# Performance work log

Hardware: AMD Instinct MI355X
Metric: run time of the kernel (lower is better)

The kernel has to match this reference:

```python
import jax, jax.numpy as jnp
import numpy as np

B, T, HID = 1, 2048, 4096
H, KVH, D = 32, 8, 128
N_REP = H // KVH
SCALE = D ** -0.5
EPS = 1e-6
THETA = 10000.0
TOPK, SINK, WIN = 256, 16, 256


def _rms_norm(x, w):
    var = jnp.mean(x * x, axis=-1, keepdims=True)
    return w * (x * jax.lax.rsqrt(var + EPS))


def _rotate_half(x):
    x1, x2 = x[..., : D // 2], x[..., D // 2 :]
    return jnp.concatenate([-x2, x1], axis=-1)


def setup_inputs() -> dict:
    key = jax.random.key(0)
    ks = jax.random.split(key, 6)
    hidden_states = jax.random.normal(ks[0], (B, T, HID), jnp.float32)
    Wq = jax.random.normal(ks[1], (HID, H * D), jnp.float32) * 0.02
    Wkv = jax.random.normal(ks[2], (HID, KVH * D), jnp.float32) * 0.02
    Wo = jax.random.normal(ks[3], (H * D, HID), jnp.float32) * 0.02
    q_norm_w = jnp.ones((D,), jnp.float32)
    k_norm_w = jnp.ones((D,), jnp.float32)
    # standard RoPE tables, theta=10000
    inv_freq = 1.0 / (THETA ** (jnp.arange(0, D, 2, dtype=jnp.float32) / D))
    freqs = jnp.arange(T, dtype=jnp.float32)[:, None] * inv_freq[None, :]  # (T, D/2)
    emb = jnp.concatenate([freqs, freqs], axis=-1)  # (T, D)
    cos = jnp.cos(emb)[None]  # (1, T, D)
    sin = jnp.sin(emb)[None]
    return {"hidden_states": hidden_states, "Wq": Wq, "Wkv": Wkv, "Wo": Wo,
            "q_norm_w": q_norm_w, "k_norm_w": k_norm_w, "cos": cos, "sin": sin}


def reference(hidden_states, Wq, Wkv, Wo, q_norm_w, k_norm_w, cos, sin):
    b, t, _ = hidden_states.shape
    s = t
    # projections -> (b, h, t, d)
    q = (hidden_states @ Wq).reshape(b, t, H, D).transpose(0, 2, 1, 3)
    kv = (hidden_states @ Wkv).reshape(b, t, KVH, D).transpose(0, 2, 1, 3)
    # qk RMSNorm per head_dim
    q = _rms_norm(q, q_norm_w)
    k = _rms_norm(kv, k_norm_w)
    v = kv  # latent KV: value shares the latent projection (no norm / rope)
    # rotary, cos/sin unsqueezed at head dim
    c = cos[:, None]  # (1,1,T,D)
    sn = sin[:, None]
    q = q * c + _rotate_half(q) * sn
    k = k * c + _rotate_half(k) * sn
    # GQA expansion
    k = jnp.repeat(k, N_REP, axis=1)
    v = jnp.repeat(v, N_REP, axis=1)
    # dense scores (reference path)
    scores = jnp.einsum("bhtd,bhsd->bhts", q, k) * SCALE  # (b,h,t,s)
    # ---- sparse DSA mask: sink | local window | per-query top-k, then causal ----
    q_idx = jnp.arange(t)
    k_idx = jnp.arange(s)
    sink = (k_idx < SINK)[None, None, None, :]
    local = (jnp.abs(q_idx[:, None] - k_idx[None, :]) <= WIN)[None, None]
    kth = jax.lax.top_k(scores, TOPK)[0][..., -1:]  # k-th largest per query
    topk_keep = scores >= kth
    causal_ok = (k_idx[None, :] <= q_idx[:, None])[None, None]
    keep = (sink | local | topk_keep) & causal_ok
    scores = jnp.where(keep, scores, -jnp.inf)
    attn = jax.nn.softmax(scores, axis=-1)
    out = jnp.einsum("bhts,bhsd->bhtd", attn, v)
    out = out.transpose(0, 2, 1, 3).reshape(b, t, H * D)
    return out @ Wo
```

## Files before the change

### kernel.cpp

```cpp
#include <hip/hip_runtime.h>
#include <hip/hip_bf16.h>

#define H 32
#define KVH 8
#define D 128
#define T 2048
#define HID 4096
#define TOPK 256
#define SINK 16
#define WIN 256
#define SCALE2 0.12753102600893415f
#define NPROJ 5120

#define SWZ(row, b) ((b) ^ (((row) & 7) << 4))

#define AS3(p) ((__attribute__((address_space(3))) void*)(p))
#define AS1(p) ((const __attribute__((address_space(1))) void*)(p))

typedef __attribute__((ext_vector_type(4))) float f32x4;
typedef __attribute__((ext_vector_type(8))) short short8;

__device__ __forceinline__ unsigned short f2bf(float f) {
  unsigned int b = __float_as_uint(f);
  b += 0x7FFFu + ((b >> 16) & 1u);
  return (unsigned short)(b >> 16);
}
__device__ __forceinline__ float bf2f(unsigned short u) {
  return __uint_as_float(((unsigned int)u) << 16);
}
__device__ __forceinline__ float ldf(const void* p, long i, bool b16) {
  return b16 ? bf2f(((const unsigned short*)p)[i]) : ((const float*)p)[i];
}
__device__ __forceinline__ bool bf16_mode(const unsigned int* probe) {
  return *probe == 0x3F803F80u;
}

__global__ void cvt_kernel(const void* __restrict__ src, unsigned short* __restrict__ dst,
                           long n, const unsigned int* probe) {
  bool b16 = bf16_mode(probe);
  long stride = (long)gridDim.x * blockDim.x;
  for (long i = (long)blockIdx.x * blockDim.x + threadIdx.x; i * 8 < n; i += stride) {
    long o = i * 8;
    if (b16) {
      *(uint4*)(dst + o) = *(const uint4*)((const unsigned short*)src + o);
    } else {
      const float* s = (const float*)src + o;
      float4 f0 = *(const float4*)s;
      float4 f1 = *(const float4*)(s + 4);
      uint4 v;
      v.x = (unsigned int)f2bf(f0.x) | ((unsigned int)f2bf(f0.y) << 16);
      v.y = (unsigned int)f2bf(f0.z) | ((unsigned int)f2bf(f0.w) << 16);
      v.z = (unsigned int)f2bf(f1.x) | ((unsigned int)f2bf(f1.y) << 16);
      v.w = (unsigned int)f2bf(f1.z) | ((unsigned int)f2bf(f1.w) << 16);
      *(uint4*)(dst + o) = v;
    }
  }
}

__global__ __launch_bounds__(256) void cvt_t(const void* __restrict__ src,
    unsigned short* __restrict__ dst, int R, int Cc, const unsigned int* probe) {
  __shared__ float tile[64][65];
  bool b16 = bf16_mode(probe);
  int r0 = blockIdx.y * 64, c0 = blockIdx.x * 64;
  int tid = threadIdx.x;
  int tr = tid >> 3;
  int tc8 = (tid & 7) * 8;
#pragma unroll
  for (int p = 0; p < 2; ++p) {
    int row = tr + p * 32;
    if (b16) {
      const unsigned short* s = (const unsigned short*)src + (size_t)(r0 + row) * Cc + c0 + tc8;
      uint4 d = *(const uint4*)s;
      const unsigned short* dv = (const unsigned short*)&d;
#pragma unroll
      for (int j = 0; j < 8; ++j) tile[row][tc8 + j] = bf2f(dv[j]);
    } else {
      const float* s = (const float*)src + (size_t)(r0 + row) * Cc + c0 + tc8;
      float4 f0 = *(const float4*)s;
      float4 f1 = *(const float4*)(s + 4);
      tile[row][tc8 + 0] = f0.x; tile[row][tc8 + 1] = f0.y;
      tile[row][tc8 + 2] = f0.z; tile[row][tc8 + 3] = f0.w;
      tile[row][tc8 + 4] = f1.x; tile[row][tc8 + 5] = f1.y;
      tile[row][tc8 + 6] = f1.z; tile[row][tc8 + 7] = f1.w;
    }
  }
  __syncthreads();
#pragma unroll
  for (int p = 0; p < 2; ++p) {
    int oc = tr + p * 32;
    unsigned short tmp[8];
#pragma unroll
    for (int j = 0; j < 8; ++j) tmp[j] = f2bf(tile[tc8 + j][oc]);
    *(uint4*)(dst + (size_t)(c0 + oc) * R + r0 + tc8) = *(uint4*)tmp;
  }
}

__global__ __launch_bounds__(256) void gemm_bf16(
    const unsigned short* __restrict__ A, const unsigned short* __restrict__ Bt,
    void* __restrict__ C, int M, int N, int K, const unsigned int* probe, int outmode) {
  __shared__ alignas(16) unsigned short As[128 * 32];
  __shared__ alignas(16) unsigned short Bs[128 * 32];
  int lin = blockIdx.x;
  int qq = (int)gridDim.x >> 3;
  int swz = (lin & 7) * qq + (lin >> 3);
  int nx = N >> 7;
  int n0 = (swz % nx) * 128, m0 = (swz / nx) * 128;
  int tid = threadIdx.x;
  int w = tid >> 6, l = tid & 63;
  int wm = (w >> 1) * 64, wn = (w & 1) * 64;
  int lr = l & 15, lg = l >> 4;

  int srow0 = (w * 2 + 0) * 16 + (l >> 2);
  int srow1 = (w * 2 + 1) * 16 + (l >> 2);
  int cch = l & 3;
  int sf0 = (srow0 ^ (srow0 >> 2)) & 3;
  int sf1 = (srow1 ^ (srow1 >> 2)) & 3;
  const unsigned short* gA0 = A + (size_t)(m0 + srow0) * K + ((cch ^ sf0) * 8);
  const unsigned short* gA1 = A + (size_t)(m0 + srow1) * K + ((cch ^ sf1) * 8);
  const unsigned short* gB0 = Bt + (size_t)(n0 + srow0) * K + ((cch ^ sf0) * 8);
  const unsigned short* gB1 = Bt + (size_t)(n0 + srow1) * K + ((cch ^ sf1) * 8);
  unsigned short* lA0 = As + (w * 2 + 0) * 16 * 32;
  unsigned short* lA1 = As + (w * 2 + 1) * 16 * 32;
  unsigned short* lB0 = Bs + (w * 2 + 0) * 16 * 32;
  unsigned short* lB1 = Bs + (w * 2 + 1) * 16 * 32;

  const unsigned short* pa[4];
  const unsigned short* pb[4];
#pragma unroll
  for (int i = 0; i < 4; ++i) {
    int ra = wm + i * 16 + lr;
    int fa = (ra ^ (ra >> 2)) & 3;
    pa[i] = As + ra * 32 + ((lg ^ fa) * 8);
    int rb = wn + i * 16 + lr;
    int fb = (rb ^ (rb >> 2)) & 3;
    pb[i] = Bs + rb * 32 + ((lg ^ fb) * 8);
  }

  f32x4 zero = {0.f, 0.f, 0.f, 0.f};
  f32x4 acc[4][4];
#pragma unroll
  for (int i = 0; i < 4; ++i)
#pragma unroll
    for (int j = 0; j < 4; ++j) acc[i][j] = zero;

  for (int k0 = 0; k0 < K; k0 += 32) {
    __builtin_amdgcn_global_load_lds(AS1(gA0 + k0), AS3(lA0), 16, 0, 0);
    __builtin_amdgcn_global_load_lds(AS1(gA1 + k0), AS3(lA1), 16, 0, 0);
    __builtin_amdgcn_global_load_lds(AS1(gB0 + k0), AS3(lB0), 16, 0, 0);
    __builtin_amdgcn_global_load_lds(AS1(gB1 + k0), AS3(lB1), 16, 0, 0);
    __syncthreads();
    short8 a[4], b[4];
#pragma unroll
    for (int i = 0; i < 4; ++i) {
      a[i] = *(const short8*)pa[i];
      b[i] = *(const short8*)pb[i];
    }
#pragma unroll
    for (int i = 0; i < 4; ++i)
#pragma unroll
      for (int j = 0; j < 4; ++j)
        acc[i][j] = __builtin_amdgcn_mfma_f32_16x16x32_bf16(a[i], b[j], acc[i][j], 0, 0, 0);
    __syncthreads();
  }
  bool b16out = (outmode == 1) || (outmode == 2 && bf16_mode(probe));
#pragma unroll
  for (int i = 0; i < 4; ++i)
#pragma unroll
    for (int j = 0; j < 4; ++j)
#pragma unroll
      for (int r = 0; r < 4; ++r) {
        int row = m0 + wm + i * 16 + lg * 4 + r;
        int col = n0 + wn + j * 16 + lr;
        float v = acc[i][j][r];
        if (b16out) ((unsigned short*)C)[(size_t)row * N + col] = f2bf(v);
        else ((float*)C)[(size_t)row * N + col] = v;
      }
}

__global__ __launch_bounds__(256) void gemm_qk(
    const unsigned short* __restrict__ Qall, const unsigned short* __restrict__ Kall,
    unsigned short* __restrict__ Sout, int h0) {
  __shared__ alignas(16) unsigned short As[128 * 32];
  __shared__ alignas(16) unsigned short Bs[128 * 32];
  int lin = blockIdx.x;
  int swz = (lin & 7) * 32 + (lin >> 3);
  int n0 = (swz & 15) * 128, m0 = (swz >> 4) * 128;
  int h = h0 + blockIdx.y;
  const unsigned short* A = Qall + (size_t)h * (T * D);
  const unsigned short* Bt = Kall + (size_t)(h >> 2) * (T * D);
  unsigned short* C = Sout + (size_t)blockIdx.y * T * T;
  int tid = threadIdx.x;
  int w = tid >> 6, l = tid & 63;
  int wm = (w >> 1) * 64, wn = (w & 1) * 64;
  int lr = l & 15, lg = l >> 4;

  int srow0 = (w * 2 + 0) * 16 + (l >> 2);
  int srow1 = (w * 2 + 1) * 16 + (l >> 2);
  int cch = l & 3;
  int sf0 = (srow0 ^ (srow0 >> 2)) & 3;
  int sf1 = (srow1 ^ (srow1 >> 2)) & 3;
  const unsigned short* gA0 = A + (size_t)(m0 + srow0) * D + ((cch ^ sf0) * 8);
  const unsigned short* gA1 = A + (size_t)(m0 + srow1) * D + ((cch ^ sf1) * 8);
  const unsigned short* gB0 = Bt + (size_t)(n0 + srow0) * D + ((cch ^ sf0) * 8);
  const unsigned short* gB1 = Bt + (size_t)(n0 + srow1) * D + ((cch ^ sf1) * 8);
  unsigned short* lA0 = As + (w * 2 + 0) * 16 * 32;
  unsigned short* lA1 = As + (w * 2 + 1) * 16 * 32;
  unsigned short* lB0 = Bs + (w * 2 + 0) * 16 * 32;
  unsigned short* lB1 = Bs + (w * 2 + 1) * 16 * 32;

  const unsigned short* pa[4];
  const unsigned short* pb[4];
#pragma unroll
  for (int i = 0; i < 4; ++i) {
    int ra = wm + i * 16 + lr;
    int fa = (ra ^ (ra >> 2)) & 3;
    pa[i] = As + ra * 32 + ((lg ^ fa) * 8);
    int rb = wn + i * 16 + lr;
    int fb = (rb ^ (rb >> 2)) & 3;
    pb[i] = Bs + rb * 32 + ((lg ^ fb) * 8);
  }

  f32x4 zero = {0.f, 0.f, 0.f, 0.f};
  f32x4 acc[4][4];
#pragma unroll
  for (int i = 0; i < 4; ++i)
#pragma unroll
    for (int j = 0; j < 4; ++j) acc[i][j] = zero;

#pragma unroll
  for (int k0 = 0; k0 < D; k0 += 32) {
    __builtin_amdgcn_global_load_lds(AS1(gA0 + k0), AS3(lA0), 16, 0, 0);
    __builtin_amdgcn_global_load_lds(AS1(gA1 + k0), AS3(lA1), 16, 0, 0);
    __builtin_amdgcn_global_load_lds(AS1(gB0 + k0), AS3(lB0), 16, 0, 0);
    __builtin_amdgcn_global_load_lds(AS1(gB1 + k0), AS3(lB1), 16, 0, 0);
    __syncthreads();
    short8 a[4], b[4];
#pragma unroll
    for (int i = 0; i < 4; ++i) {
      a[i] = *(const short8*)pa[i];
      b[i] = *(const short8*)pb[i];
    }
#pragma unroll
    for (int i = 0; i < 4; ++i)
#pragma unroll
      for (int j = 0; j < 4; ++j)
        acc[i][j] = __builtin_amdgcn_mfma_f32_16x16x32_bf16(a[i], b[j], acc[i][j], 0, 0, 0);
    __syncthreads();
  }
#pragma unroll
  for (int i = 0; i < 4; ++i)
#pragma unroll
    for (int j = 0; j < 4; ++j)
#pragma unroll
      for (int r = 0; r < 4; ++r) {
        int row = m0 + wm + i * 16 + lg * 4 + r;
        int col = n0 + wn + j * 16 + lr;
        C[(size_t)row * T + col] = f2bf(acc[i][j][r]);
      }
}

__global__ __launch_bounds__(256) void qk_prep(
    const unsigned short* __restrict__ Proj, const void* nw, const void* cosp, const void* sinp,
    unsigned short* __restrict__ Qh, const unsigned int* probe) {
  bool b16 = bf16_mode(probe);
  int w = threadIdx.x >> 6, l = threadIdx.x & 63;
  int gw = blockIdx.x * 4 + w;
  int t = gw >> 5, h = gw & 31;
  const unsigned short* x = Proj + (size_t)t * NPROJ + h * D;
  float x1 = bf2f(x[l]), x2 = bf2f(x[l + 64]);
  float s = x1 * x1 + x2 * x2;
  for (int m = 32; m; m >>= 1) s += __shfl_xor(s, m);
  float inv = rsqrtf(s * (1.0f / D) + 1e-6f);
  float w1 = ldf(nw, l, b16), w2 = ldf(nw, l + 64, b16);
  float c1 = ldf(cosp, (long)t * D + l, b16), c2 = ldf(cosp, (long)t * D + l + 64, b16);
  float s1 = ldf(sinp, (long)t * D + l, b16), s2 = ldf(sinp, (long)t * D + l + 64, b16);
  float xn1 = x1 * inv * w1, xn2 = x2 * inv * w2;
  unsigned short* o = Qh + (size_t)h * T * D + (size_t)t * D;
  o[l] = f2bf(SCALE2 * (xn1 * c1 - xn2 * s1));
  o[l + 64] = f2bf(SCALE2 * (xn2 * c2 + xn1 * s2));
}

__global__ __launch_bounds__(256) void kv_prep(
    const unsigned short* __restrict__ Proj, const void* nw, const void* cosp, const void* sinp,
    unsigned short* __restrict__ Kh, unsigned short* __restrict__ Vt, const unsigned int* probe) {
  bool b16 = bf16_mode(probe);
  int w = threadIdx.x >> 6, l = threadIdx.x & 63;
  int gw = blockIdx.x * 4 + w;
  int t = gw >> 3, h = gw & 7;
  const unsigned short* x = Proj + (size_t)t * NPROJ + (H * D) + h * D;
  float x1 = bf2f(x[l]), x2 = bf2f(x[l + 64]);
  Vt[(size_t)h * D * T + (size_t)l * T + t] = x[l];
  Vt[(size_t)h * D * T + (size_t)(l + 64) * T + t] = x[l + 64];
  float s = x1 * x1 + x2 * x2;
  for (int m = 32; m; m >>= 1) s += __shfl_xor(s, m);
  float inv = rsqrtf(s * (1.0f / D) + 1e-6f);
  float w1 = ldf(nw, l, b16), w2 = ldf(nw, l + 64, b16);
  float c1 = ldf(cosp, (long)t * D + l, b16), c2 = ldf(cosp, (long)t * D + l + 64, b16);
  float s1 = ldf(sinp, (long)t * D + l, b16), s2 = ldf(sinp, (long)t * D + l + 64, b16);
  float xn1 = x1 * inv * w1, xn2 = x2 * inv * w2;
  unsigned short* o = Kh + (size_t)h * T * D + (size_t)t * D;
  o[l] = f2bf(xn1 * c1 - xn2 * s1);
  o[l + 64] = f2bf(xn2 * c2 + xn1 * s2);
}

__global__ __launch_bounds__(1024, 8) void attn_sm(
    const unsigned short* __restrict__ S,
    const unsigned short* __restrict__ Vt, unsigned short* __restrict__ attn_out, int h0) {
  __shared__ alignas(16) unsigned short sc[16][2048];
  __shared__ alignas(16) float part[8][64][4];
  __shared__ float zinv[16];
  int t0 = blockIdx.x * 16;
  int h = h0 + blockIdx.y;
  int hk = h >> 2;
  int tid = threadIdx.x;
  int w = tid >> 6, l = tid & 63;
  int lr = l & 15, lg = l >> 4;
  f32x4 zero = {0.f, 0.f, 0.f, 0.f};
  char* scB = (char*)sc;

  {
    int row = w, tq = t0 + row;
    int rsw = (row & 7) << 4;
    int lim = (t0 + 15) >> 7;
    char* rb = scB + row * 4096;
    const unsigned int* Sr = (const unsigned int*)(S + ((size_t)blockIdx.y * T + tq) * T);
#pragma unroll
    for (int i = 0; i < 16; ++i)
      *(unsigned int*)(rb + ((256 * i + 4 * l) ^ rsw)) = Sr[l + 64 * i];
    unsigned int klo[16], khi[16];
#pragma unroll
    for (int i = 0; i < 16; ++i) {
      unsigned int b = *(const unsigned int*)(rb + ((256 * i + 4 * l) ^ rsw));
      unsigned int m = (b >> 15) & 0x00010001u;
      unsigned int kk2 = b ^ (0x80008000u | (m * 0x7FFFu));
      klo[i] = kk2 & 0xFFFFu;
      khi[i] = kk2 >> 16;
    }
    unsigned int um = 0;
#pragma unroll
    for (int i = 0; i < 16; ++i) {
      unsigned int a_ = klo[i] > khi[i] ? klo[i] : khi[i];
      um = um > a_ ? um : a_;
    }
    for (int m = 32; m; m >>= 1) {
      unsigned int o = (unsigned int)__shfl_xor((int)um, m);
      um = um > o ? um : o;
    }
    unsigned int lo = 0, hi = um;
    {
      unsigned int mid = um > 192u ? um - 192u : 1u;
      int cnt = 0;
#pragma unroll
      for (int i = 0; i < 16; ++i)
        cnt += (int)__popcll(__ballot(klo[i] >= mid)) + (int)__popcll(__ballot(khi[i] >= mid));
      if (cnt >= TOPK) lo = mid; else hi = mid - 1u;
    }
    if (lo == 0u && um > 1024u) {
      unsigned int mid = um - 1024u;
      int cnt = 0;
#pragma unroll
      for (int i = 0; i < 16; ++i)
        cnt += (int)__popcll(__ballot(klo[i] >= mid)) + (int)__popcll(__ballot(khi[i] >= mid));
      if (cnt >= TOPK) lo = mid; else hi = mid - 1u;
    }
    while (lo < hi) {
      unsigned int mid = (lo + hi + 1u) >> 1;
      int cnt = 0;
#pragma unroll
      for (int i = 0; i < 16; ++i)
        cnt += (int)__popcll(__ballot(klo[i] >= mid)) + (int)__popcll(__ballot(khi[i] >= mid));
      if (cnt >= TOPK) lo = mid; else hi = mid - 1u;
    }
    unsigned int thr = lo;

    int ca0 = (tq - 2 * l) >> 7;
    int ca1 = (tq - 2 * l - 1) >> 7;
    int wa0 = (tq - WIN - 2 * l + 127) >> 7;
    int wa1 = (tq - WIN - 2 * l - 1 + 127) >> 7;
    bool snk = (l < 8);
    unsigned int mA = 0, mB = 0, mk = 0;
#pragma unroll
    for (int i = 0; i < 16; ++i) {
      if (i > lim) break;
      bool k0 = (i <= ca0) && (((i == 0) && snk) || (i >= wa0) || (klo[i] >= thr));
      bool k1 = (i <= ca1) && (((i == 0) && snk) || (i >= wa1) || (khi[i] >= thr));
      if (k0) { mA |= (1u << i); mk = mk > klo[i] ? mk : klo[i]; }
      if (k1) { mB |= (1u << i); mk = mk > khi[i] ? mk : khi[i]; }
    }
    for (int m = 32; m; m >>= 1) {
      unsigned int o = (unsigned int)__shfl_xor((int)mk, m);
      mk = mk > o ? mk : o;
    }
    unsigned int mb = (mk & 0x8000u) ? (mk ^ 0x8000u) : ((~mk) & 0xFFFFu);
    float mx = bf2f((unsigned short)mb);

    float z = 0.f;
#pragma unroll
    for (int i = 0; i < 16; ++i) {
      if (i > lim) break;
      unsigned int b0 = (klo[i] & 0x8000u) ? (klo[i] ^ 0x8000u) : ((~klo[i]) & 0xFFFFu);
      unsigned int b1 = (khi[i] & 0x8000u) ? (khi[i] ^ 0x8000u) : ((~khi[i]) & 0xFFFFu);
      float x0 = bf2f((unsigned short)b0) - mx;
      float x1 = bf2f((unsigned short)b1) - mx;
      float e0x, e1x;
      asm("v_exp_f32 %0, %1" : "=v"(e0x) : "v"(x0));
      asm("v_exp_f32 %0, %1" : "=v"(e1x) : "v"(x1));
      float e0 = ((mA >> i) & 1u) ? e0x : 0.f;
      float e1 = ((mB >> i) & 1u) ? e1x : 0.f;
      z += e0 + e1;
      *(unsigned int*)(rb + ((256 * i + 4 * l) ^ rsw)) =
          (unsigned int)f2bf(e0) | ((unsigned int)f2bf(e1) << 16);
    }
    for (int m = 32; m; m >>= 1) z += __shfl_xor(z, m);
    if (l == 0) zinv[row] = 1.0f / z;
  }
  __syncthreads();

  {
    int half = w >> 3;
    int d0 = (w & 7) * 16;
    const unsigned short* Vb = Vt + (size_t)hk * (D * T) + (size_t)(d0 + lr) * T + lg * 8;
    const char* prb = scB + lr * 4096;
    int psw = (lr & 7) << 4;
    f32x4 o0 = zero, o1 = zero;
    int ks_end = (t0 + 47) >> 5;
    int ks_endE = (ks_end + 1) & ~1;
    int kmid = ((ks_endE >> 1) + 1) & ~1;
    int ksA = half ? kmid : 0;
    int ksB = half ? ks_endE : kmid;
    short8 vb0 = *(const short8*)(Vb + ksA * 32);
    short8 vb1 = *(const short8*)(Vb + (ksA + 1) * 32);
#pragma unroll 2
    for (int ks = ksA; ks < ksB; ks += 2) {
      int kn = (ks + 2 < ksB) ? (ks + 2) : ks;
      short8 pa0 = *(const short8*)(prb + ((ks * 64 + lg * 16) ^ psw));
      __builtin_amdgcn_s_setprio(1);
      o0 = __builtin_amdgcn_mfma_f32_16x16x32_bf16(vb0, pa0, o0, 0, 0, 0);
      __builtin_amdgcn_s_setprio(0);
      vb0 = *(const short8*)(Vb + kn * 32);
      short8 pa1 = *(const short8*)(prb + (((ks + 1) * 64 + lg * 16) ^ psw));
      __builtin_amdgcn_s_setprio(1);
      o1 = __builtin_amdgcn_mfma_f32_16x16x32_bf16(vb1, pa1, o1, 0, 0, 0);
      __builtin_amdgcn_s_setprio(0);
      vb1 = *(const short8*)(Vb + (kn + 1) * 32);
    }
    f32x4 oo;
#pragma unroll
    for (int r = 0; r < 4; ++r) oo[r] = o0[r] + o1[r];
    if (half) *(f32x4*)(&part[w & 7][l][0]) = oo;
    __syncthreads();
    if (!half) {
      f32x4 po = *(const f32x4*)(&part[w & 7][l][0]);
      float rz = zinv[lr];
      unsigned short tmp[4];
#pragma unroll
      for (int r = 0; r < 4; ++r) tmp[r] = f2bf((oo[r] + po[r]) * rz);
      unsigned short* dst = attn_out + (size_t)(t0 + lr) * (H * D) + h * D + d0 + lg * 4;
      *(uint2*)dst = *(uint2*)tmp;
    }
  }
}

extern "C" void kernel_launch(void* const* d_in, const int* in_sizes, int n_in,
                              void* d_out, int out_size, void* d_ws, size_t ws_size,
                              hipStream_t stream) {
  (void)in_sizes; (void)n_in; (void)out_size;
  const void* hs = d_in[0];
  const void* Wq = d_in[1];
  const void* Wkv = d_in[2];
  const void* Wo = d_in[3];
  const unsigned int* probe = (const unsigned int*)d_in[4];
  const void* knw = d_in[5];
  const void* cosp = d_in[6];
  const void* sinp = d_in[7];

  char* ws = (char*)d_ws;
  unsigned short* WqT_bf = (unsigned short*)(ws);
  unsigned short* WkvT_bf= (unsigned short*)(ws + 33554432);
  unsigned short* WoT_bf = (unsigned short*)(ws + 41943040);
  unsigned short* hid_bf = (unsigned short*)(ws + 75497472);
  unsigned short* Proj_bf= (unsigned short*)(ws + 92274688);
  unsigned short* Qh     = (unsigned short*)(ws + 134217728);
  unsigned short* Kh     = (unsigned short*)(ws + 150994944);
  unsigned short* Vt     = (unsigned short*)(ws + 155189248);
  unsigned short* attn_bf= (unsigned short*)(ws + 159383552);
  const size_t S_off = 176160768;
  const size_t HEAD_S = (size_t)T * T * 2;

  hipLaunchKernelGGL(cvt_kernel, dim3(1024), dim3(256), 0, stream, hs, hid_bf, (long)T * HID, probe);
  hipLaunchKernelGGL(cvt_t, dim3(64, 64), dim3(256), 0, stream, Wq, WqT_bf, HID, H * D, probe);
  hipLaunchKernelGGL(cvt_t, dim3(16, 64), dim3(256), 0, stream, Wkv, WkvT_bf, HID, KVH * D, probe);
  hipLaunchKernelGGL(cvt_t, dim3(64, 64), dim3(256), 0, stream, Wo, WoT_bf, H * D, HID, probe);

  hipLaunchKernelGGL(gemm_bf16, dim3(640), dim3(256), 0, stream,
                     hid_bf, WqT_bf, (void*)Proj_bf, 2048, NPROJ, 4096,
                     (const unsigned int*)nullptr, 1);

  hipLaunchKernelGGL(qk_prep, dim3(16384), dim3(256), 0, stream, Proj_bf, d_in[4], cosp, sinp, Qh, probe);
  hipLaunchKernelGGL(kv_prep, dim3(4096), dim3(256), 0, stream, Proj_bf, knw, cosp, sinp, Kh, Vt, probe);

  size_t tail = (ws_size > S_off) ? (ws_size - S_off) / HEAD_S : 0;
  unsigned short* Sbuf;
  int cap;
  if (tail >= 6) {
    Sbuf = (unsigned short*)(ws + S_off);
    cap = (int)(tail < (size_t)H ? tail : (size_t)H);
  } else {
    Sbuf = (unsigned short*)ws;
    cap = 5;
  }
  for (int h0 = 0; h0 < H; h0 += cap) {
    int cnt = (H - h0 < cap) ? (H - h0) : cap;
    hipLaunchKernelGGL(gemm_qk, dim3(256, cnt), dim3(256), 0, stream, Qh, Kh, Sbuf, h0);
    hipLaunchKernelGGL(attn_sm, dim3(128, cnt), dim3(1024), 0, stream, Sbuf, Vt, attn_bf, h0);
  }

  hipLaunchKernelGGL(gemm_bf16, dim3(512), dim3(256), 0, stream,
                     attn_bf, WoT_bf, d_out, 2048, 4096, 4096, probe, 2);
}
```

Before: 722.3 us.

## Split-K by two for projection GEMMs with fp32 partials and reduce kernel

Both the QKV projection GEMM and the output projection GEMM now split K in half across a second grid dimension. Each half writes fp32 partial tiles to workspace, and a new reduce kernel sums the two halves and converts to bf16 or fp32 output. The aim is more blocks per GEMM to improve CU occupancy and wave balance. The cost is writing and re-reading large fp32 partial buffers, plus two extra launches, and workspace regions are reused to hold them.

```diff
diff --git a/kernel.cpp b/kernel.cpp
--- a/kernel.cpp
+++ b/kernel.cpp
@@ -57,6 +57,27 @@
   }
 }
 
+__global__ void reduce2(const float* __restrict__ A, const float* __restrict__ B,
+                        long n, void* __restrict__ out, const unsigned int* probe, int outmode) {
+  bool b16out = (outmode == 1) || (outmode == 2 && bf16_mode(probe));
+  long stride = (long)gridDim.x * blockDim.x;
+  for (long i = (long)blockIdx.x * blockDim.x + threadIdx.x; i * 4 < n; i += stride) {
+    long o = i * 4;
+    float4 a = *(const float4*)(A + o);
+    float4 b = *(const float4*)(B + o);
+    float4 s;
+    s.x = a.x + b.x; s.y = a.y + b.y; s.z = a.z + b.z; s.w = a.w + b.w;
+    if (b16out) {
+      uint2 v;
+      v.x = (unsigned int)f2bf(s.x) | ((unsigned int)f2bf(s.y) << 16);
+      v.y = (unsigned int)f2bf(s.z) | ((unsigned int)f2bf(s.w) << 16);
+      *(uint2*)((unsigned short*)out + o) = v;
+    } else {
+      *(float4*)((float*)out + o) = s;
+    }
+  }
+}
+
 __global__ __launch_bounds__(256) void cvt_t(const void* __restrict__ src,
     unsigned short* __restrict__ dst, int R, int Cc, const unsigned int* probe) {
   __shared__ float tile[64][65];
@@ -95,9 +116,9 @@
   }
 }
 
-__global__ __launch_bounds__(256) void gemm_bf16(
+__global__ __launch_bounds__(256) void gemm_splitk(
     const unsigned short* __restrict__ A, const unsigned short* __restrict__ Bt,
-    void* __restrict__ C, int M, int N, int K, const unsigned int* probe, int outmode) {
+    float* __restrict__ P, int M, int N, int K) {
   __shared__ alignas(16) unsigned short As[128 * 32];
   __shared__ alignas(16) unsigned short Bs[128 * 32];
   int lin = blockIdx.x;
@@ -105,6 +126,10 @@
   int swz = (lin & 7) * qq + (lin >> 3);
   int nx = N >> 7;
   int n0 = (swz % nx) * 128, m0 = (swz / nx) * 128;
+  int kslice = blockIdx.y;
+  int kh = K >> 1;
+  int kbase = kslice * kh;
+  float* C = P + (size_t)kslice * M * N;
   int tid = threadIdx.x;
   int w = tid >> 6, l = tid & 63;
   int wm = (w >> 1) * 64, wn = (w & 1) * 64;
@@ -115,10 +140,10 @@
   int cch = l & 3;
   int sf0 = (srow0 ^ (srow0 >> 2)) & 3;
   int sf1 = (srow1 ^ (srow1 >> 2)) & 3;
-  const unsigned short* gA0 = A + (size_t)(m0 + srow0) * K + ((cch ^ sf0) * 8);
-  const unsigned short* gA1 = A + (size_t)(m0 + srow1) * K + ((cch ^ sf1) * 8);
-  const unsigned short* gB0 = Bt + (size_t)(n0 + srow0) * K + ((cch ^ sf0) * 8);
-  const unsigned short* gB1 = Bt + (size_t)(n0 + srow1) * K + ((cch ^ sf1) * 8);
+  const unsigned short* gA0 = A + (size_t)(m0 + srow0) * K + kbase + ((cch ^ sf0) * 8);
+  const unsigned short* gA1 = A + (size_t)(m0 + srow1) * K + kbase + ((cch ^ sf1) * 8);
+  const unsigned short* gB0 = Bt + (size_t)(n0 + srow0) * K + kbase + ((cch ^ sf0) * 8);
+  const unsigned short* gB1 = Bt + (size_t)(n0 + srow1) * K + kbase + ((cch ^ sf1) * 8);
   unsigned short* lA0 = As + (w * 2 + 0) * 16 * 32;
   unsigned short* lA1 = As + (w * 2 + 1) * 16 * 32;
   unsigned short* lB0 = Bs + (w * 2 + 0) * 16 * 32;
@@ -143,7 +168,7 @@
 #pragma unroll
     for (int j = 0; j < 4; ++j) acc[i][j] = zero;
 
-  for (int k0 = 0; k0 < K; k0 += 32) {
+  for (int k0 = 0; k0 < kh; k0 += 32) {
     __builtin_amdgcn_global_load_lds(AS1(gA0 + k0), AS3(lA0), 16, 0, 0);
     __builtin_amdgcn_global_load_lds(AS1(gA1 + k0), AS3(lA1), 16, 0, 0);
     __builtin_amdgcn_global_load_lds(AS1(gB0 + k0), AS3(lB0), 16, 0, 0);
@@ -162,7 +187,6 @@
         acc[i][j] = __builtin_amdgcn_mfma_f32_16x16x32_bf16(a[i], b[j], acc[i][j], 0, 0, 0);
     __syncthreads();
   }
-  bool b16out = (outmode == 1) || (outmode == 2 && bf16_mode(probe));
 #pragma unroll
   for (int i = 0; i < 4; ++i)
 #pragma unroll
@@ -171,9 +195,7 @@
       for (int r = 0; r < 4; ++r) {
         int row = m0 + wm + i * 16 + lg * 4 + r;
         int col = n0 + wn + j * 16 + lr;
-        float v = acc[i][j][r];
-        if (b16out) ((unsigned short*)C)[(size_t)row * N + col] = f2bf(v);
-        else ((float*)C)[(size_t)row * N + col] = v;
+        C[(size_t)row * N + col] = acc[i][j][r];
       }
 }
 
@@ -479,11 +501,13 @@
   unsigned short* WkvT_bf= (unsigned short*)(ws + 33554432);
   unsigned short* WoT_bf = (unsigned short*)(ws + 41943040);
   unsigned short* hid_bf = (unsigned short*)(ws + 75497472);
-  unsigned short* Proj_bf= (unsigned short*)(ws + 92274688);
+  float*          projP  = (float*)(ws + 92274688);
+  unsigned short* Proj_bf= (unsigned short*)(ws);
   unsigned short* Qh     = (unsigned short*)(ws + 134217728);
   unsigned short* Kh     = (unsigned short*)(ws + 150994944);
   unsigned short* Vt     = (unsigned short*)(ws + 155189248);
   unsigned short* attn_bf= (unsigned short*)(ws + 159383552);
+  float*          outP   = (float*)(ws + 92274688);
   const size_t S_off = 176160768;
   const size_t HEAD_S = (size_t)T * T * 2;
 
@@ -492,9 +516,11 @@
   hipLaunchKernelGGL(cvt_t, dim3(16, 64), dim3(256), 0, stream, Wkv, WkvT_bf, HID, KVH * D, probe);
   hipLaunchKernelGGL(cvt_t, dim3(64, 64), dim3(256), 0, stream, Wo, WoT_bf, H * D, HID, probe);
 
-  hipLaunchKernelGGL(gemm_bf16, dim3(640), dim3(256), 0, stream,
-                     hid_bf, WqT_bf, (void*)Proj_bf, 2048, NPROJ, 4096,
-                     (const unsigned int*)nullptr, 1);
+  hipLaunchKernelGGL(gemm_splitk, dim3(640, 2), dim3(256), 0, stream,
+                     hid_bf, WqT_bf, projP, 2048, NPROJ, 4096);
+  hipLaunchKernelGGL(reduce2, dim3(4096), dim3(256), 0, stream,
+                     projP, projP + (size_t)2048 * NPROJ, (long)2048 * NPROJ,
+                     (void*)Proj_bf, probe, 1);
 
   hipLaunchKernelGGL(qk_prep, dim3(16384), dim3(256), 0, stream, Proj_bf, d_in[4], cosp, sinp, Qh, probe);
   hipLaunchKernelGGL(kv_prep, dim3(4096), dim3(256), 0, stream, Proj_bf, knw, cosp, sinp, Kh, Vt, probe);
@@ -515,6 +541,8 @@
     hipLaunchKernelGGL(attn_sm, dim3(128, cnt), dim3(1024), 0, stream, Sbuf, Vt, attn_bf, h0);
   }
 
-  hipLaunchKernelGGL(gemm_bf16, dim3(512), dim3(256), 0, stream,
-                     attn_bf, WoT_bf, d_out, 2048, 4096, 4096, probe, 2);
-}
+  hipLaunchKernelGGL(gemm_splitk, dim3(512, 2), dim3(256), 0, stream,
+                     attn_bf, WoT_bf, outP, 2048, 4096, 4096);
+  hipLaunchKernelGGL(reduce2, dim3(4096), dim3(256), 0, stream,
+                     outP, outP + (size_t)2048 * 4096, (long)2048 * 4096, d_out, probe, 2);
+}
```

New measurement: 778.0 us. 1.08x slower.
